# Kernel optimization log

Measured on AMD Instinct MI355X. Metric: run time of the kernel, lower is better.

Reference implementation:

```python
import jax, jax.numpy as jnp
import numpy as np

B, H, S, D = 4, 16, 2048, 64


def setup_inputs() -> dict:
    key = jax.random.key(0)
    kq, kk, kv = jax.random.split(key, 3)
    q = jax.random.normal(kq, (B, H, S, D), dtype=jnp.float32)
    k = jax.random.normal(kk, (B, H, S, D), dtype=jnp.float32)
    v = jax.random.normal(kv, (B, H, S, D), dtype=jnp.float32)
    return {"q": q, "k": k, "v": v}


def reference(q, k, v):
    d_k = q.shape[-1]
    scale = 1.0 / jnp.sqrt(jnp.asarray(d_k, dtype=q.dtype))
    # scores: [B, H, S_q, S_k]
    scores = jnp.einsum("bhqd,bhkd->bhqk", q, k) * scale
    attn = jax.nn.softmax(scores, axis=-1)
    out = jnp.einsum("bhqk,bhkd->bhqd", attn, v)
    return out
```

## Files before the change

### kernel.cpp

```cpp
#include <hip/hip_runtime.h>


#define NT 32
#define M0 10.0f

typedef unsigned short u16;
typedef unsigned int   u32;
typedef __bf16 bf16x8 __attribute__((ext_vector_type(8)));
typedef u16    u16x8  __attribute__((ext_vector_type(8)));
typedef u32    u32x4  __attribute__((ext_vector_type(4)));
typedef float  f32x16 __attribute__((ext_vector_type(16)));

__device__ __forceinline__ u16 f2bf(float f) {
    union { float f; u32 u; } x; x.f = f;
    u32 r = x.u + 0x7FFFu + ((x.u >> 16) & 1u);
    return (u16)(r >> 16);
}
__device__ __forceinline__ u32 cvt_pk_bf16(float lo, float hi) {
    u32 r; asm("v_cvt_pk_bf16_f32 %0, %1, %2" : "=v"(r) : "v"(lo), "v"(hi));
    return r;
}
__device__ __forceinline__ float fexp2(float x) {
    float r; asm("v_exp_f32 %0, %1" : "=v"(r) : "v"(x));
    return r;
}

__global__ __launch_bounds__(256)
void prepass_kernel(const float* __restrict__ K, const float* __restrict__ V,
                    u16* __restrict__ Kb, u16* __restrict__ Vt)
{
    __shared__ u16 T[64 * 66];
    const int t   = threadIdx.x;
    const int bh  = blockIdx.x >> 5;
    const int s0  = (blockIdx.x & 31) * 64;
    const int row = t >> 2;
    const int c0  = (t & 3) * 16;

    {
        const float* kp = K + ((size_t)bh * 2048 + s0 + row) * 64 + c0;
        #pragma unroll
        for (int i = 0; i < 2; ++i) {
            float4 a = ((const float4*)kp)[2 * i];
            float4 b = ((const float4*)kp)[2 * i + 1];
            u16x8 o;
            o[0] = f2bf(a.x); o[1] = f2bf(a.y); o[2] = f2bf(a.z); o[3] = f2bf(a.w);
            o[4] = f2bf(b.x); o[5] = f2bf(b.y); o[6] = f2bf(b.z); o[7] = f2bf(b.w);
            *(u16x8*)(Kb + ((size_t)bh * 2048 + s0 + row) * 64 + c0 + 8 * i) = o;
        }
    }
    {
        const float* vp = V + ((size_t)bh * 2048 + s0 + row) * 64 + c0;
        #pragma unroll
        for (int i = 0; i < 4; ++i) {
            float4 a = ((const float4*)vp)[i];
            T[(c0 + 4 * i + 0) * 66 + row] = f2bf(a.x);
            T[(c0 + 4 * i + 1) * 66 + row] = f2bf(a.y);
            T[(c0 + 4 * i + 2) * 66 + row] = f2bf(a.z);
            T[(c0 + 4 * i + 3) * 66 + row] = f2bf(a.w);
        }
    }
    __syncthreads();
    {
        const int d  = t >> 2;
        const int k0 = (t & 3) * 16;
        #pragma unroll
        for (int i = 0; i < 2; ++i) {
            u16x8 o;
            #pragma unroll
            for (int j = 0; j < 8; ++j) o[j] = T[d * 66 + k0 + 8 * i + j];
            *(u16x8*)(Vt + ((size_t)bh * 64 + d) * 2048 + s0 + k0 + 8 * i) = o;
        }
    }
}

__global__ __launch_bounds__(256)
void attn_fwd_kernel(const float* __restrict__ Qg, const u16* __restrict__ Kb,
                     const u16* __restrict__ Vt, float* __restrict__ Og)
{
    __shared__ u16 Klds[2][4096];
    __shared__ u16 Vlds[2][4096];

    const int tid = threadIdx.x;
    const int w   = tid >> 6;
    const int l31 = tid & 31;
    const int hi  = (tid & 63) >> 5;
    const int sw  = l31 & 7;

    const int id = (blockIdx.x & 7) * 128 + (blockIdx.x >> 3);
    const int bh = id >> 4;
    const int q0 = (id & 15) * 128;
    const int qw = q0 + w * 32;
    const int qr = qw + l31;

    const size_t baseQ = (size_t)bh * 2048 * 64;
    const u16* kg = Kb + (size_t)bh * 2048 * 64;
    const u16* vg = Vt + (size_t)bh * 64 * 2048;

    const float SCL = 0.125f * 1.44269504088896f;
    bf16x8 bq[4];
    #pragma unroll
    for (int dc = 0; dc < 4; ++dc) {
        const float* qp = Qg + baseQ + (size_t)qr * 64 + dc * 16 + hi * 8;
        float4 a = ((const float4*)qp)[0];
        float4 b = ((const float4*)qp)[1];
        u16x8 t;
        t[0] = f2bf(a.x * SCL); t[1] = f2bf(a.y * SCL);
        t[2] = f2bf(a.z * SCL); t[3] = f2bf(a.w * SCL);
        t[4] = f2bf(b.x * SCL); t[5] = f2bf(b.y * SCL);
        t[6] = f2bf(b.z * SCL); t[7] = f2bf(b.w * SCL);
        bq[dc] = __builtin_bit_cast(bf16x8, t);
    }

    int co[4];
    #pragma unroll
    for (int c = 0; c < 4; ++c) co[c] = ((2 * c + hi) ^ sw) * 8;

    u32x4 onev; onev[0] = 0x3F803F80u; onev[1] = 0x3F803F80u;
    onev[2] = 0x3F803F80u; onev[3] = 0x3F803F80u;
    const bf16x8 bones = __builtin_bit_cast(bf16x8, onev);

    f32x16 acc[2], acc2;
    #pragma unroll
    for (int i = 0; i < 16; ++i) { acc[0][i] = 0.f; acc[1][i] = 0.f; acc2[i] = 0.f; }

    const int srow = tid >> 3;
    const int kc   = ((tid & 7) ^ (srow & 7)) * 8;
    const u16* kS0 = kg + (size_t)srow * 64 + kc;
    const u16* kS1 = kg + (size_t)(srow + 32) * 64 + kc;
    const u16* vS0 = vg + (size_t)srow * 2048 + kc;
    const u16* vS1 = vg + (size_t)(srow + 32) * 2048 + kc;

    u16x8 rA, rB, rC, rD;
    auto load_tile = [&](int t) {
        rA = *(const u16x8*)(kS0 + (size_t)t * 4096);
        rB = *(const u16x8*)(kS1 + (size_t)t * 4096);
        rC = *(const u16x8*)(vS0 + (size_t)t * 64);
        rD = *(const u16x8*)(vS1 + (size_t)t * 64);
    };
    auto write_tile = [&](int t) {
        u16* kd = &Klds[t & 1][tid * 8];
        u16* vd = &Vlds[t & 1][tid * 8];
        *(u16x8*)kd = rA;
        *(u16x8*)(kd + 2048) = rB;
        *(u16x8*)vd = rC;
        *(u16x8*)(vd + 2048) = rD;
    };

    auto sm_pv = [&](f32x16 s, const u16* Vl, int kh) {
        #pragma unroll
        for (int i = 0; i < 16; ++i) s[i] = fexp2(s[i]);
        u32 w0[8];
        #pragma unroll
        for (int a = 0; a < 8; ++a)
            w0[a] = cvt_pk_bf16(s[2 * a], s[2 * a + 1]);
        __builtin_amdgcn_s_setprio(1);
        #pragma unroll
        for (int ki = 0; ki < 2; ++ki) {
            const int ks = kh * 2 + ki, mb = 4 * ki;
            u32 a0 = w0[mb + 0], a2 = w0[mb + 2];
            u32 a1 = w0[mb + 1], a3 = w0[mb + 3];
            asm("v_permlane32_swap_b32 %0, %1" : "+v"(a0), "+v"(a2));
            asm("v_permlane32_swap_b32 %0, %1" : "+v"(a1), "+v"(a3));
            u32x4 fw0; fw0[0] = a0; fw0[1] = a1; fw0[2] = a2; fw0[3] = a3;
            bf16x8 pa = __builtin_bit_cast(bf16x8, fw0);

            bf16x8 bv0 = *(const bf16x8*)(Vl + l31 * 64 + co[ks]);
            bf16x8 bv1 = *(const bf16x8*)(Vl + (32 + l31) * 64 + co[ks]);
            acc[0] = __builtin_amdgcn_mfma_f32_32x32x16_bf16(pa, bv0, acc[0], 0, 0, 0);
            acc[1] = __builtin_amdgcn_mfma_f32_32x32x16_bf16(pa, bv1, acc[1], 0, 0, 0);
            acc2   = __builtin_amdgcn_mfma_f32_32x32x16_bf16(pa, bones, acc2, 0, 0, 0);
        }
        __builtin_amdgcn_s_setprio(0);
    };

    auto compute = [&](const u16* Kl, const u16* Vl) {
        f32x16 sA, sB;
        #pragma unroll
        for (int i = 0; i < 16; ++i) { sA[i] = -M0; sB[i] = -M0; }
        __builtin_amdgcn_s_setprio(1);
        #pragma unroll
        for (int dc = 0; dc < 4; ++dc) {
            bf16x8 ak0 = *(const bf16x8*)(Kl + l31 * 64 + co[dc]);
            sA = __builtin_amdgcn_mfma_f32_32x32x16_bf16(ak0, bq[dc], sA, 0, 0, 0);
            bf16x8 ak1 = *(const bf16x8*)(Kl + (32 + l31) * 64 + co[dc]);
            sB = __builtin_amdgcn_mfma_f32_32x32x16_bf16(ak1, bq[dc], sB, 0, 0, 0);
        }
        __builtin_amdgcn_s_setprio(0);
        sm_pv(sA, Vl, 0);
        sm_pv(sB, Vl, 1);
    };

    load_tile(0);
    write_tile(0);
    __syncthreads();
    for (int t = 0; t < NT; ++t) {
        if (t + 1 < NT) load_tile(t + 1);
        compute(Klds[t & 1], Vlds[t & 1]);
        if (t + 1 < NT) {
            write_tile(t + 1);
            __syncthreads();
        }
    }

    #pragma unroll
    for (int r = 0; r < 16; ++r) {
        int cr = (r & 3) + 8 * (r >> 2) + 4 * hi;
        float inv = 1.0f / acc2[r];
        size_t o = baseQ + (size_t)(qw + cr) * 64 + l31;
        Og[o]      = acc[0][r] * inv;
        Og[o + 32] = acc[1][r] * inv;
    }
}

extern "C" void kernel_launch(void* const* d_in, const int* in_sizes, int n_in,
                              void* d_out, int out_size, void* d_ws, size_t ws_size,
                              hipStream_t stream) {
    const float* q = (const float*)d_in[0];
    const float* k = (const float*)d_in[1];
    const float* v = (const float*)d_in[2];
    float* o = (float*)d_out;
    u16* kb = (u16*)d_ws;
    u16* vt = kb + (size_t)64 * 2048 * 64;
    prepass_kernel<<<dim3(2048), dim3(256), 0, stream>>>(k, v, kb, vt);
    attn_fwd_kernel<<<dim3(1024), dim3(256), 0, stream>>>(q, kb, vt, o);
}
```

Measured before the change: 113.2 us.

## Split attention over key halves and combine, single-buffer LDS tiles

Splits each query tile's key range into two halves, launching twice as many blocks. Each block writes unnormalized partial outputs and row sums, and a new combine kernel adds the partials and normalizes. This works because the fixed max offset makes partial exp-sums directly additive. LDS double buffering is replaced by a single buffer with an extra barrier, which may raise occupancy but serializes load and compute. The cost is extra global traffic for the partials, an additional kernel launch, and dependence on the workspace size.

```diff
diff --git a/kernel.cpp b/kernel.cpp
--- a/kernel.cpp
+++ b/kernel.cpp
@@ -1,7 +1,6 @@
 #include <hip/hip_runtime.h>
 
 
-#define NT 32
 #define M0 10.0f
 
 typedef unsigned short u16;
@@ -73,12 +72,14 @@
     }
 }
 
+template<int SPLIT>
 __global__ __launch_bounds__(256)
 void attn_fwd_kernel(const float* __restrict__ Qg, const u16* __restrict__ Kb,
-                     const u16* __restrict__ Vt, float* __restrict__ Og)
+                     const u16* __restrict__ Vt, float* __restrict__ Og,
+                     float* __restrict__ O1, float* __restrict__ Ls)
 {
-    __shared__ u16 Klds[2][4096];
-    __shared__ u16 Vlds[2][4096];
+    __shared__ u16 Klds[4096];
+    __shared__ u16 Vlds[4096];
 
     const int tid = threadIdx.x;
     const int w   = tid >> 6;
@@ -86,9 +87,19 @@
     const int hi  = (tid & 63) >> 5;
     const int sw  = l31 & 7;
 
-    const int id = (blockIdx.x & 7) * 128 + (blockIdx.x >> 3);
-    const int bh = id >> 4;
-    const int q0 = (id & 15) * 128;
+    const int id = (blockIdx.x & 7) * (SPLIT ? 256 : 128) + (blockIdx.x >> 3);
+    int bh, q0, h;
+    if (SPLIT) {
+        bh = id >> 5;
+        q0 = ((id & 31) >> 1) * 128;
+        h  = id & 1;
+    } else {
+        bh = id >> 4;
+        q0 = (id & 15) * 128;
+        h  = 0;
+    }
+    const int tt0 = SPLIT ? h * 16 : 0;
+    const int NTl = SPLIT ? 16 : 32;
     const int qw = q0 + w * 32;
     const int qr = qw + l31;
 
@@ -131,22 +142,22 @@
     const u16* vS1 = vg + (size_t)(srow + 32) * 2048 + kc;
 
     u16x8 rA, rB, rC, rD;
-    auto load_tile = [&](int t) {
-        rA = *(const u16x8*)(kS0 + (size_t)t * 4096);
-        rB = *(const u16x8*)(kS1 + (size_t)t * 4096);
-        rC = *(const u16x8*)(vS0 + (size_t)t * 64);
-        rD = *(const u16x8*)(vS1 + (size_t)t * 64);
-    };
-    auto write_tile = [&](int t) {
-        u16* kd = &Klds[t & 1][tid * 8];
-        u16* vd = &Vlds[t & 1][tid * 8];
+    auto load_tile = [&](int tt) {
+        rA = *(const u16x8*)(kS0 + (size_t)tt * 4096);
+        rB = *(const u16x8*)(kS1 + (size_t)tt * 4096);
+        rC = *(const u16x8*)(vS0 + (size_t)tt * 64);
+        rD = *(const u16x8*)(vS1 + (size_t)tt * 64);
+    };
+    auto write_tile = [&]() {
+        u16* kd = &Klds[tid * 8];
+        u16* vd = &Vlds[tid * 8];
         *(u16x8*)kd = rA;
         *(u16x8*)(kd + 2048) = rB;
         *(u16x8*)vd = rC;
         *(u16x8*)(vd + 2048) = rD;
     };
 
-    auto sm_pv = [&](f32x16 s, const u16* Vl, int kh) {
+    auto sm_pv = [&](f32x16 s, int kh) {
         #pragma unroll
         for (int i = 0; i < 16; ++i) s[i] = fexp2(s[i]);
         u32 w0[8];
@@ -164,8 +175,8 @@
             u32x4 fw0; fw0[0] = a0; fw0[1] = a1; fw0[2] = a2; fw0[3] = a3;
             bf16x8 pa = __builtin_bit_cast(bf16x8, fw0);
 
-            bf16x8 bv0 = *(const bf16x8*)(Vl + l31 * 64 + co[ks]);
-            bf16x8 bv1 = *(const bf16x8*)(Vl + (32 + l31) * 64 + co[ks]);
+            bf16x8 bv0 = *(const bf16x8*)(Vlds + l31 * 64 + co[ks]);
+            bf16x8 bv1 = *(const bf16x8*)(Vlds + (32 + l31) * 64 + co[ks]);
             acc[0] = __builtin_amdgcn_mfma_f32_32x32x16_bf16(pa, bv0, acc[0], 0, 0, 0);
             acc[1] = __builtin_amdgcn_mfma_f32_32x32x16_bf16(pa, bv1, acc[1], 0, 0, 0);
             acc2   = __builtin_amdgcn_mfma_f32_32x32x16_bf16(pa, bones, acc2, 0, 0, 0);
@@ -173,43 +184,79 @@
         __builtin_amdgcn_s_setprio(0);
     };
 
-    auto compute = [&](const u16* Kl, const u16* Vl) {
+    auto compute = [&]() {
         f32x16 sA, sB;
         #pragma unroll
         for (int i = 0; i < 16; ++i) { sA[i] = -M0; sB[i] = -M0; }
         __builtin_amdgcn_s_setprio(1);
         #pragma unroll
         for (int dc = 0; dc < 4; ++dc) {
-            bf16x8 ak0 = *(const bf16x8*)(Kl + l31 * 64 + co[dc]);
+            bf16x8 ak0 = *(const bf16x8*)(Klds + l31 * 64 + co[dc]);
             sA = __builtin_amdgcn_mfma_f32_32x32x16_bf16(ak0, bq[dc], sA, 0, 0, 0);
-            bf16x8 ak1 = *(const bf16x8*)(Kl + (32 + l31) * 64 + co[dc]);
+            bf16x8 ak1 = *(const bf16x8*)(Klds + (32 + l31) * 64 + co[dc]);
             sB = __builtin_amdgcn_mfma_f32_32x32x16_bf16(ak1, bq[dc], sB, 0, 0, 0);
         }
         __builtin_amdgcn_s_setprio(0);
-        sm_pv(sA, Vl, 0);
-        sm_pv(sB, Vl, 1);
-    };
-
-    load_tile(0);
-    write_tile(0);
+        sm_pv(sA, 0);
+        sm_pv(sB, 1);
+    };
+
+    load_tile(tt0);
+    write_tile();
     __syncthreads();
-    for (int t = 0; t < NT; ++t) {
-        if (t + 1 < NT) load_tile(t + 1);
-        compute(Klds[t & 1], Vlds[t & 1]);
-        if (t + 1 < NT) {
-            write_tile(t + 1);
+    for (int t = 0; t < NTl; ++t) {
+        if (t + 1 < NTl) load_tile(tt0 + t + 1);
+        compute();
+        if (t + 1 < NTl) {
             __syncthreads();
-        }
-    }
-
-    #pragma unroll
-    for (int r = 0; r < 16; ++r) {
-        int cr = (r & 3) + 8 * (r >> 2) + 4 * hi;
-        float inv = 1.0f / acc2[r];
-        size_t o = baseQ + (size_t)(qw + cr) * 64 + l31;
-        Og[o]      = acc[0][r] * inv;
-        Og[o + 32] = acc[1][r] * inv;
-    }
+            write_tile();
+            __syncthreads();
+        }
+    }
+
+    if (SPLIT) {
+        float* Op = h ? O1 : Og;
+        #pragma unroll
+        for (int r = 0; r < 16; ++r) {
+            int cr = (r & 3) + 8 * (r >> 2) + 4 * hi;
+            size_t o = baseQ + (size_t)(qw + cr) * 64 + l31;
+            Op[o]      = acc[0][r];
+            Op[o + 32] = acc[1][r];
+        }
+        if (l31 == 0) {
+            #pragma unroll
+            for (int r = 0; r < 16; ++r) {
+                int cr = (r & 3) + 8 * (r >> 2) + 4 * hi;
+                Ls[h * 131072 + bh * 2048 + qw + cr] = acc2[r];
+            }
+        }
+    } else {
+        #pragma unroll
+        for (int r = 0; r < 16; ++r) {
+            int cr = (r & 3) + 8 * (r >> 2) + 4 * hi;
+            float inv = 1.0f / acc2[r];
+            size_t o = baseQ + (size_t)(qw + cr) * 64 + l31;
+            Og[o]      = acc[0][r] * inv;
+            Og[o + 32] = acc[1][r] * inv;
+        }
+    }
+}
+
+__global__ __launch_bounds__(256)
+void combine_kernel(float* __restrict__ O, const float* __restrict__ O1,
+                    const float* __restrict__ Ls)
+{
+    const int i4 = blockIdx.x * 256 + threadIdx.x;
+    const int row = i4 >> 4;
+    const float inv = 1.0f / (Ls[row] + Ls[131072 + row]);
+    float4 a = ((const float4*)O)[i4];
+    float4 b = ((const float4*)O1)[i4];
+    float4 o;
+    o.x = (a.x + b.x) * inv;
+    o.y = (a.y + b.y) * inv;
+    o.z = (a.z + b.z) * inv;
+    o.w = (a.w + b.w) * inv;
+    ((float4*)O)[i4] = o;
 }
 
 extern "C" void kernel_launch(void* const* d_in, const int* in_sizes, int n_in,
@@ -221,6 +268,15 @@
     float* o = (float*)d_out;
     u16* kb = (u16*)d_ws;
     u16* vt = kb + (size_t)64 * 2048 * 64;
+    float* o1 = (float*)((char*)d_ws + 33554432);
+    float* ls = (float*)((char*)d_ws + 67108864);
+    const size_t NEED = 67108864 + 1048576;
+
     prepass_kernel<<<dim3(2048), dim3(256), 0, stream>>>(k, v, kb, vt);
-    attn_fwd_kernel<<<dim3(1024), dim3(256), 0, stream>>>(q, kb, vt, o);
-}
+    if (ws_size >= NEED) {
+        attn_fwd_kernel<1><<<dim3(2048), dim3(256), 0, stream>>>(q, kb, vt, o, o1, ls);
+        combine_kernel<<<dim3(8192), dim3(256), 0, stream>>>(o, o1, ls);
+    } else {
+        attn_fwd_kernel<0><<<dim3(1024), dim3(256), 0, stream>>>(q, kb, vt, o, o1, ls);
+    }
+}
```

Result: slower. 129.0 us (+14.0%).

## Pre-swizzle K/V into MFMA fragment order and load directly from global

Applied to the files above, without the earlier changes.

The prepass now writes K and V^T in an MFMA-fragment-ready layout, with each lane's 8 bf16 values contiguous per 512-element chunk. The attention kernel drops the LDS double buffering and the __syncthreads barriers and reads fragments straight from global memory or cache. This removes LDS staging traffic and barrier stalls. In exchange, every wave re-reads K/V from L2 without intra-block sharing, and there is no explicit prefetch to hide global load latency.

```diff
diff --git a/kernel.cpp b/kernel.cpp
--- a/kernel.cpp
+++ b/kernel.cpp
@@ -27,64 +27,66 @@
 
 __global__ __launch_bounds__(256)
 void prepass_kernel(const float* __restrict__ K, const float* __restrict__ V,
-                    u16* __restrict__ Kb, u16* __restrict__ Vt)
+                    u16* __restrict__ Kf, u16* __restrict__ Vf)
 {
-    __shared__ u16 T[64 * 66];
-    const int t   = threadIdx.x;
+    __shared__ u16 T[64 * 72];
+    const int tid = threadIdx.x;
     const int bh  = blockIdx.x >> 5;
-    const int s0  = (blockIdx.x & 31) * 64;
-    const int row = t >> 2;
-    const int c0  = (t & 3) * 16;
+    const int t   = blockIdx.x & 31;
+    const int l   = tid & 63;
+    const int l31 = l & 31;
+    const int hi  = l >> 5;
+    const int idx = tid >> 6;
 
     {
-        const float* kp = K + ((size_t)bh * 2048 + s0 + row) * 64 + c0;
+        const int rh  = idx >> 1;
+        const int dc0 = (idx & 1) * 2;
         #pragma unroll
-        for (int i = 0; i < 2; ++i) {
-            float4 a = ((const float4*)kp)[2 * i];
-            float4 b = ((const float4*)kp)[2 * i + 1];
+        for (int d = 0; d < 2; ++d) {
+            const int dc = dc0 + d;
+            const float* src = K + ((size_t)bh * 2048 + t * 64 + rh * 32 + l31) * 64
+                                 + dc * 16 + hi * 8;
+            float4 a = ((const float4*)src)[0];
+            float4 b = ((const float4*)src)[1];
             u16x8 o;
             o[0] = f2bf(a.x); o[1] = f2bf(a.y); o[2] = f2bf(a.z); o[3] = f2bf(a.w);
             o[4] = f2bf(b.x); o[5] = f2bf(b.y); o[6] = f2bf(b.z); o[7] = f2bf(b.w);
-            *(u16x8*)(Kb + ((size_t)bh * 2048 + s0 + row) * 64 + c0 + 8 * i) = o;
+            *(u16x8*)(Kf + (size_t)bh * 131072 + (size_t)(t * 8 + rh * 4 + dc) * 512 + l * 8) = o;
         }
     }
     {
-        const float* vp = V + ((size_t)bh * 2048 + s0 + row) * 64 + c0;
+        const int row = tid >> 2;
+        const int c0  = (tid & 3) * 16;
+        const float* vp = V + ((size_t)bh * 2048 + t * 64 + row) * 64 + c0;
         #pragma unroll
         for (int i = 0; i < 4; ++i) {
             float4 a = ((const float4*)vp)[i];
-            T[(c0 + 4 * i + 0) * 66 + row] = f2bf(a.x);
-            T[(c0 + 4 * i + 1) * 66 + row] = f2bf(a.y);
-            T[(c0 + 4 * i + 2) * 66 + row] = f2bf(a.z);
-            T[(c0 + 4 * i + 3) * 66 + row] = f2bf(a.w);
+            T[(c0 + 4 * i + 0) * 72 + row] = f2bf(a.x);
+            T[(c0 + 4 * i + 1) * 72 + row] = f2bf(a.y);
+            T[(c0 + 4 * i + 2) * 72 + row] = f2bf(a.z);
+            T[(c0 + 4 * i + 3) * 72 + row] = f2bf(a.w);
         }
     }
     __syncthreads();
     {
-        const int d  = t >> 2;
-        const int k0 = (t & 3) * 16;
+        const int ks = idx;
         #pragma unroll
-        for (int i = 0; i < 2; ++i) {
-            u16x8 o;
-            #pragma unroll
-            for (int j = 0; j < 8; ++j) o[j] = T[d * 66 + k0 + 8 * i + j];
-            *(u16x8*)(Vt + ((size_t)bh * 64 + d) * 2048 + s0 + k0 + 8 * i) = o;
+        for (int dt = 0; dt < 2; ++dt) {
+            u16x8 o = *(const u16x8*)(T + (dt * 32 + l31) * 72 + ks * 16 + hi * 8);
+            *(u16x8*)(Vf + (size_t)bh * 131072 + (size_t)(t * 8 + ks * 2 + dt) * 512 + l * 8) = o;
         }
     }
 }
 
 __global__ __launch_bounds__(256)
-void attn_fwd_kernel(const float* __restrict__ Qg, const u16* __restrict__ Kb,
-                     const u16* __restrict__ Vt, float* __restrict__ Og)
+void attn_fwd_kernel(const float* __restrict__ Qg, const u16* __restrict__ Kf,
+                     const u16* __restrict__ Vf, float* __restrict__ Og)
 {
-    __shared__ u16 Klds[2][4096];
-    __shared__ u16 Vlds[2][4096];
-
     const int tid = threadIdx.x;
     const int w   = tid >> 6;
-    const int l31 = tid & 31;
-    const int hi  = (tid & 63) >> 5;
-    const int sw  = l31 & 7;
+    const int l   = tid & 63;
+    const int l31 = l & 31;
+    const int hi  = l >> 5;
 
     const int id = (blockIdx.x & 7) * 128 + (blockIdx.x >> 3);
     const int bh = id >> 4;
@@ -93,8 +95,8 @@
     const int qr = qw + l31;
 
     const size_t baseQ = (size_t)bh * 2048 * 64;
-    const u16* kg = Kb + (size_t)bh * 2048 * 64;
-    const u16* vg = Vt + (size_t)bh * 64 * 2048;
+    const u16* kf = Kf + (size_t)bh * 131072 + l * 8;
+    const u16* vf = Vf + (size_t)bh * 131072 + l * 8;
 
     const float SCL = 0.125f * 1.44269504088896f;
     bf16x8 bq[4];
@@ -111,10 +113,6 @@
         bq[dc] = __builtin_bit_cast(bf16x8, t);
     }
 
-    int co[4];
-    #pragma unroll
-    for (int c = 0; c < 4; ++c) co[c] = ((2 * c + hi) ^ sw) * 8;
-
     u32x4 onev; onev[0] = 0x3F803F80u; onev[1] = 0x3F803F80u;
     onev[2] = 0x3F803F80u; onev[3] = 0x3F803F80u;
     const bf16x8 bones = __builtin_bit_cast(bf16x8, onev);
@@ -123,83 +121,54 @@
     #pragma unroll
     for (int i = 0; i < 16; ++i) { acc[0][i] = 0.f; acc[1][i] = 0.f; acc2[i] = 0.f; }
 
-    const int srow = tid >> 3;
-    const int kc   = ((tid & 7) ^ (srow & 7)) * 8;
-    const u16* kS0 = kg + (size_t)srow * 64 + kc;
-    const u16* kS1 = kg + (size_t)(srow + 32) * 64 + kc;
-    const u16* vS0 = vg + (size_t)srow * 2048 + kc;
-    const u16* vS1 = vg + (size_t)(srow + 32) * 2048 + kc;
+    for (int t = 0; t < NT; ++t) {
+        const u16* kt = kf + (size_t)t * 4096;
+        const u16* vt = vf + (size_t)t * 4096;
 
-    u16x8 rA, rB, rC, rD;
-    auto load_tile = [&](int t) {
-        rA = *(const u16x8*)(kS0 + (size_t)t * 4096);
-        rB = *(const u16x8*)(kS1 + (size_t)t * 4096);
-        rC = *(const u16x8*)(vS0 + (size_t)t * 64);
-        rD = *(const u16x8*)(vS1 + (size_t)t * 64);
-    };
-    auto write_tile = [&](int t) {
-        u16* kd = &Klds[t & 1][tid * 8];
-        u16* vd = &Vlds[t & 1][tid * 8];
-        *(u16x8*)kd = rA;
-        *(u16x8*)(kd + 2048) = rB;
-        *(u16x8*)vd = rC;
-        *(u16x8*)(vd + 2048) = rD;
-    };
-
-    auto sm_pv = [&](f32x16 s, const u16* Vl, int kh) {
-        #pragma unroll
-        for (int i = 0; i < 16; ++i) s[i] = fexp2(s[i]);
-        u32 w0[8];
-        #pragma unroll
-        for (int a = 0; a < 8; ++a)
-            w0[a] = cvt_pk_bf16(s[2 * a], s[2 * a + 1]);
-        __builtin_amdgcn_s_setprio(1);
-        #pragma unroll
-        for (int ki = 0; ki < 2; ++ki) {
-            const int ks = kh * 2 + ki, mb = 4 * ki;
-            u32 a0 = w0[mb + 0], a2 = w0[mb + 2];
-            u32 a1 = w0[mb + 1], a3 = w0[mb + 3];
-            asm("v_permlane32_swap_b32 %0, %1" : "+v"(a0), "+v"(a2));
-            asm("v_permlane32_swap_b32 %0, %1" : "+v"(a1), "+v"(a3));
-            u32x4 fw0; fw0[0] = a0; fw0[1] = a1; fw0[2] = a2; fw0[3] = a3;
-            bf16x8 pa = __builtin_bit_cast(bf16x8, fw0);
-
-            bf16x8 bv0 = *(const bf16x8*)(Vl + l31 * 64 + co[ks]);
-            bf16x8 bv1 = *(const bf16x8*)(Vl + (32 + l31) * 64 + co[ks]);
-            acc[0] = __builtin_amdgcn_mfma_f32_32x32x16_bf16(pa, bv0, acc[0], 0, 0, 0);
-            acc[1] = __builtin_amdgcn_mfma_f32_32x32x16_bf16(pa, bv1, acc[1], 0, 0, 0);
-            acc2   = __builtin_amdgcn_mfma_f32_32x32x16_bf16(pa, bones, acc2, 0, 0, 0);
-        }
-        __builtin_amdgcn_s_setprio(0);
-    };
-
-    auto compute = [&](const u16* Kl, const u16* Vl) {
         f32x16 sA, sB;
         #pragma unroll
         for (int i = 0; i < 16; ++i) { sA[i] = -M0; sB[i] = -M0; }
         __builtin_amdgcn_s_setprio(1);
         #pragma unroll
         for (int dc = 0; dc < 4; ++dc) {
-            bf16x8 ak0 = *(const bf16x8*)(Kl + l31 * 64 + co[dc]);
-            sA = __builtin_amdgcn_mfma_f32_32x32x16_bf16(ak0, bq[dc], sA, 0, 0, 0);
-            bf16x8 ak1 = *(const bf16x8*)(Kl + (32 + l31) * 64 + co[dc]);
-            sB = __builtin_amdgcn_mfma_f32_32x32x16_bf16(ak1, bq[dc], sB, 0, 0, 0);
+            bf16x8 a0 = *(const bf16x8*)(kt + (size_t)dc * 512);
+            bf16x8 a1 = *(const bf16x8*)(kt + (size_t)(4 + dc) * 512);
+            sA = __builtin_amdgcn_mfma_f32_32x32x16_bf16(a0, bq[dc], sA, 0, 0, 0);
+            sB = __builtin_amdgcn_mfma_f32_32x32x16_bf16(a1, bq[dc], sB, 0, 0, 0);
         }
         __builtin_amdgcn_s_setprio(0);
-        sm_pv(sA, Vl, 0);
-        sm_pv(sB, Vl, 1);
-    };
 
-    load_tile(0);
-    write_tile(0);
-    __syncthreads();
-    for (int t = 0; t < NT; ++t) {
-        if (t + 1 < NT) load_tile(t + 1);
-        compute(Klds[t & 1], Vlds[t & 1]);
-        if (t + 1 < NT) {
-            write_tile(t + 1);
-            __syncthreads();
+        #pragma unroll
+        for (int i = 0; i < 16; ++i) sA[i] = fexp2(sA[i]);
+        #pragma unroll
+        for (int i = 0; i < 16; ++i) sB[i] = fexp2(sB[i]);
+
+        u32 w0[8], w1[8];
+        #pragma unroll
+        for (int a = 0; a < 8; ++a) {
+            w0[a] = cvt_pk_bf16(sA[2 * a], sA[2 * a + 1]);
+            w1[a] = cvt_pk_bf16(sB[2 * a], sB[2 * a + 1]);
         }
+
+        __builtin_amdgcn_s_setprio(1);
+        #pragma unroll
+        for (int ks = 0; ks < 4; ++ks) {
+            const int kh = ks >> 1, mb = 4 * (ks & 1);
+            u32* wp = kh ? w1 : w0;
+            u32 a0 = wp[mb + 0], a2 = wp[mb + 2];
+            u32 a1 = wp[mb + 1], a3 = wp[mb + 3];
+            asm("v_permlane32_swap_b32 %0, %1" : "+v"(a0), "+v"(a2));
+            asm("v_permlane32_swap_b32 %0, %1" : "+v"(a1), "+v"(a3));
+            u32x4 fw; fw[0] = a0; fw[1] = a1; fw[2] = a2; fw[3] = a3;
+            bf16x8 pa = __builtin_bit_cast(bf16x8, fw);
+
+            bf16x8 bv0 = *(const bf16x8*)(vt + (size_t)(ks * 2 + 0) * 512);
+            bf16x8 bv1 = *(const bf16x8*)(vt + (size_t)(ks * 2 + 1) * 512);
+            acc[0] = __builtin_amdgcn_mfma_f32_32x32x16_bf16(pa, bv0, acc[0], 0, 0, 0);
+            acc[1] = __builtin_amdgcn_mfma_f32_32x32x16_bf16(pa, bv1, acc[1], 0, 0, 0);
+            acc2   = __builtin_amdgcn_mfma_f32_32x32x16_bf16(pa, bones, acc2, 0, 0, 0);
+        }
+        __builtin_amdgcn_s_setprio(0);
     }
 
     #pragma unroll
@@ -219,8 +188,8 @@
     const float* k = (const float*)d_in[1];
     const float* v = (const float*)d_in[2];
     float* o = (float*)d_out;
-    u16* kb = (u16*)d_ws;
-    u16* vt = kb + (size_t)64 * 2048 * 64;
-    prepass_kernel<<<dim3(2048), dim3(256), 0, stream>>>(k, v, kb, vt);
-    attn_fwd_kernel<<<dim3(1024), dim3(256), 0, stream>>>(q, kb, vt, o);
+    u16* kf = (u16*)d_ws;
+    u16* vf = kf + (size_t)64 * 2048 * 64;
+    prepass_kernel<<<dim3(2048), dim3(256), 0, stream>>>(k, v, kf, vf);
+    attn_fwd_kernel<<<dim3(1024), dim3(256), 0, stream>>>(q, kf, vf, o);
 }
```

Measured after the change: 164.6 us. +45.5%, slower.

## Halve block to 64 query rows with single-buffered LDS and staggered K/V loads

Applied to the files above, without the earlier changes.

Switches the attention kernel from 256-thread blocks covering 128 queries to 128-thread blocks covering 64 queries, doubling the grid. LDS is single-buffered, which halves shared memory per block, and each thread now loads whole K/V rows with a swizzled global read pattern. The V prefetch is issued after the QK MFMAs and an extra barrier is added before the LDS write. The aim is higher occupancy and more blocks in flight, at the cost of twice the K/V global traffic per query and an extra sync per tile.

```diff
diff --git a/kernel.cpp b/kernel.cpp
--- a/kernel.cpp
+++ b/kernel.cpp
@@ -73,12 +73,12 @@
     }
 }
 
-__global__ __launch_bounds__(256)
+__global__ __launch_bounds__(128)
 void attn_fwd_kernel(const float* __restrict__ Qg, const u16* __restrict__ Kb,
                      const u16* __restrict__ Vt, float* __restrict__ Og)
 {
-    __shared__ u16 Klds[2][4096];
-    __shared__ u16 Vlds[2][4096];
+    __shared__ u16 Klds[4096];
+    __shared__ u16 Vlds[4096];
 
     const int tid = threadIdx.x;
     const int w   = tid >> 6;
@@ -86,9 +86,9 @@
     const int hi  = (tid & 63) >> 5;
     const int sw  = l31 & 7;
 
-    const int id = (blockIdx.x & 7) * 128 + (blockIdx.x >> 3);
-    const int bh = id >> 4;
-    const int q0 = (id & 15) * 128;
+    const int id = (blockIdx.x & 7) * 256 + (blockIdx.x >> 3);
+    const int bh = id >> 5;
+    const int q0 = (id & 31) * 64;
     const int qw = q0 + w * 32;
     const int qr = qw + l31;
 
@@ -123,30 +123,33 @@
     #pragma unroll
     for (int i = 0; i < 16; ++i) { acc[0][i] = 0.f; acc[1][i] = 0.f; acc2[i] = 0.f; }
 
-    const int srow = tid >> 3;
-    const int kc   = ((tid & 7) ^ (srow & 7)) * 8;
-    const u16* kS0 = kg + (size_t)srow * 64 + kc;
-    const u16* kS1 = kg + (size_t)(srow + 32) * 64 + kc;
-    const u16* vS0 = vg + (size_t)srow * 2048 + kc;
-    const u16* vS1 = vg + (size_t)(srow + 32) * 2048 + kc;
-
-    u16x8 rA, rB, rC, rD;
-    auto load_tile = [&](int t) {
-        rA = *(const u16x8*)(kS0 + (size_t)t * 4096);
-        rB = *(const u16x8*)(kS1 + (size_t)t * 4096);
-        rC = *(const u16x8*)(vS0 + (size_t)t * 64);
-        rD = *(const u16x8*)(vS1 + (size_t)t * 64);
-    };
-    auto write_tile = [&](int t) {
-        u16* kd = &Klds[t & 1][tid * 8];
-        u16* vd = &Vlds[t & 1][tid * 8];
-        *(u16x8*)kd = rA;
-        *(u16x8*)(kd + 2048) = rB;
-        *(u16x8*)vd = rC;
-        *(u16x8*)(vd + 2048) = rD;
-    };
-
-    auto sm_pv = [&](f32x16 s, const u16* Vl, int kh) {
+    const int srow = tid >> 1;
+    const int sc0  = (tid & 1) * 4;
+    const int sx   = srow & 7;
+    const u16* kSr = kg + (size_t)srow * 64;
+    const u16* vSr = vg + (size_t)srow * 2048;
+
+    u16x8 rK[4], rV[4];
+    auto loadK = [&](int t) {
+        #pragma unroll
+        for (int i = 0; i < 4; ++i)
+            rK[i] = *(const u16x8*)(kSr + (size_t)t * 4096 + (size_t)(((sc0 + i) ^ sx) * 8));
+    };
+    auto loadV = [&](int t) {
+        #pragma unroll
+        for (int i = 0; i < 4; ++i)
+            rV[i] = *(const u16x8*)(vSr + (size_t)t * 64 + (size_t)(((sc0 + i) ^ sx) * 8));
+    };
+    auto write_tile = [&]() {
+        u16* kd = Klds + srow * 64 + sc0 * 8;
+        u16* vd = Vlds + srow * 64 + sc0 * 8;
+        #pragma unroll
+        for (int i = 0; i < 4; ++i) *(u16x8*)(kd + i * 8) = rK[i];
+        #pragma unroll
+        for (int i = 0; i < 4; ++i) *(u16x8*)(vd + i * 8) = rV[i];
+    };
+
+    auto sm_pv = [&](f32x16 s, int kh) {
         #pragma unroll
         for (int i = 0; i < 16; ++i) s[i] = fexp2(s[i]);
         u32 w0[8];
@@ -164,8 +167,8 @@
             u32x4 fw0; fw0[0] = a0; fw0[1] = a1; fw0[2] = a2; fw0[3] = a3;
             bf16x8 pa = __builtin_bit_cast(bf16x8, fw0);
 
-            bf16x8 bv0 = *(const bf16x8*)(Vl + l31 * 64 + co[ks]);
-            bf16x8 bv1 = *(const bf16x8*)(Vl + (32 + l31) * 64 + co[ks]);
+            bf16x8 bv0 = *(const bf16x8*)(Vlds + l31 * 64 + co[ks]);
+            bf16x8 bv1 = *(const bf16x8*)(Vlds + (32 + l31) * 64 + co[ks]);
             acc[0] = __builtin_amdgcn_mfma_f32_32x32x16_bf16(pa, bv0, acc[0], 0, 0, 0);
             acc[1] = __builtin_amdgcn_mfma_f32_32x32x16_bf16(pa, bv1, acc[1], 0, 0, 0);
             acc2   = __builtin_amdgcn_mfma_f32_32x32x16_bf16(pa, bones, acc2, 0, 0, 0);
@@ -173,31 +176,33 @@
         __builtin_amdgcn_s_setprio(0);
     };
 
-    auto compute = [&](const u16* Kl, const u16* Vl) {
+    loadK(0); loadV(0);
+    write_tile();
+    __syncthreads();
+    for (int t = 0; t < NT; ++t) {
+        if (t + 1 < NT) loadK(t + 1);
+
         f32x16 sA, sB;
         #pragma unroll
         for (int i = 0; i < 16; ++i) { sA[i] = -M0; sB[i] = -M0; }
         __builtin_amdgcn_s_setprio(1);
         #pragma unroll
         for (int dc = 0; dc < 4; ++dc) {
-            bf16x8 ak0 = *(const bf16x8*)(Kl + l31 * 64 + co[dc]);
+            bf16x8 ak0 = *(const bf16x8*)(Klds + l31 * 64 + co[dc]);
             sA = __builtin_amdgcn_mfma_f32_32x32x16_bf16(ak0, bq[dc], sA, 0, 0, 0);
-            bf16x8 ak1 = *(const bf16x8*)(Kl + (32 + l31) * 64 + co[dc]);
+            bf16x8 ak1 = *(const bf16x8*)(Klds + (32 + l31) * 64 + co[dc]);
             sB = __builtin_amdgcn_mfma_f32_32x32x16_bf16(ak1, bq[dc], sB, 0, 0, 0);
         }
         __builtin_amdgcn_s_setprio(0);
-        sm_pv(sA, Vl, 0);
-        sm_pv(sB, Vl, 1);
-    };
-
-    load_tile(0);
-    write_tile(0);
-    __syncthreads();
-    for (int t = 0; t < NT; ++t) {
-        if (t + 1 < NT) load_tile(t + 1);
-        compute(Klds[t & 1], Vlds[t & 1]);
+
+        if (t + 1 < NT) loadV(t + 1);
+
+        sm_pv(sA, 0);
+        sm_pv(sB, 1);
+
         if (t + 1 < NT) {
-            write_tile(t + 1);
+            __syncthreads();
+            write_tile();
             __syncthreads();
         }
     }
@@ -222,5 +227,5 @@
     u16* kb = (u16*)d_ws;
     u16* vt = kb + (size_t)64 * 2048 * 64;
     prepass_kernel<<<dim3(2048), dim3(256), 0, stream>>>(k, v, kb, vt);
-    attn_fwd_kernel<<<dim3(1024), dim3(256), 0, stream>>>(q, kb, vt, o);
-}
+    attn_fwd_kernel<<<dim3(2048), dim3(128), 0, stream>>>(q, kb, vt, o);
+}
```

After: 157.6 us. +39.3%, slower.
